# Optimization experiments

Hardware: AMD Instinct MI355X
Metric: run time of the kernel (lower is better)

Reference implementation:

```python
import jax, jax.numpy as jnp
import numpy as np

B, S, D_MODEL = 2, 2048, 2048
H, KVH, HD = 32, 8, 64
N_REP = H // KVH
EPS = 1e-6


def _rope_tables(seq_len, head_dim):
    pos = np.arange(seq_len, dtype=np.float32)
    inv_freq = 1.0 / (10000.0 ** (np.arange(0, head_dim, 2, dtype=np.float32) / head_dim))
    freqs = pos[:, None] * inv_freq[None, :]           # [S, HD/2]
    emb = np.concatenate([freqs, freqs], axis=-1)      # [S, HD]
    return jnp.asarray(np.cos(emb)), jnp.asarray(np.sin(emb))


def setup_inputs() -> dict:
    key = jax.random.key(0)
    ks = jax.random.split(key, 6)
    x = jax.random.normal(ks[0], (B, S, D_MODEL), jnp.float32)
    rope_cos, rope_sin = _rope_tables(S, HD)
    sc_in = 1.0 / np.sqrt(D_MODEL).astype(np.float32)
    sc_o = 1.0 / np.sqrt(H * HD).astype(np.float32)
    Wq = jax.random.normal(ks[1], (H * HD, D_MODEL), jnp.float32) * sc_in
    Wk = jax.random.normal(ks[2], (KVH * HD, D_MODEL), jnp.float32) * sc_in
    Wv = jax.random.normal(ks[3], (KVH * HD, D_MODEL), jnp.float32) * sc_in
    Wo = jax.random.normal(ks[4], (D_MODEL, H * HD), jnp.float32) * sc_o
    q_norm_w = jnp.ones((HD,), jnp.float32)
    k_norm_w = jnp.ones((HD,), jnp.float32)
    return dict(x=x, rope_cos=rope_cos, rope_sin=rope_sin, Wq=Wq, Wk=Wk, Wv=Wv,
                Wo=Wo, q_norm_w=q_norm_w, k_norm_w=k_norm_w)


def _rms_norm(x, w):
    return x * jax.lax.rsqrt(jnp.mean(x * x, axis=-1, keepdims=True) + EPS) * w


def _rotate_half(x):
    x1, x2 = jnp.split(x, 2, axis=-1)
    return jnp.concatenate((-x2, x1), axis=-1)


def reference(x, rope_cos, rope_sin, Wq, Wk, Wv, Wo, q_norm_w, k_norm_w):
    b, s, _ = x.shape
    q = (x @ Wq.T).reshape(b, s, H, HD)
    k = (x @ Wk.T).reshape(b, s, KVH, HD)
    v = (x @ Wv.T).reshape(b, s, KVH, HD)
    # per-head QK RMSNorm
    q = _rms_norm(q, q_norm_w)
    k = _rms_norm(k, k_norm_w)
    # RoPE: cos/sin [S, HD] -> broadcast over heads
    cos = rope_cos[:, None, :]
    sin = rope_sin[:, None, :]
    q = q * cos + _rotate_half(q) * sin
    k = k * cos + _rotate_half(k) * sin
    # GQA: repeat_interleave KV heads
    k = jnp.repeat(k, N_REP, axis=2)
    v = jnp.repeat(v, N_REP, axis=2)
    q = q.transpose(0, 2, 1, 3)  # [B,H,S,HD]
    k = k.transpose(0, 2, 1, 3)
    v = v.transpose(0, 2, 1, 3)
    scale = np.float32(1.0 / np.sqrt(HD))
    scores = jnp.einsum('bhqd,bhkd->bhqk', q, k) * scale
    causal = jnp.tril(jnp.ones((s, s), dtype=bool))
    scores = jnp.where(causal, scores, jnp.finfo(scores.dtype).min)
    attn = jax.nn.softmax(scores, axis=-1)
    out = jnp.einsum('bhqk,bhkd->bhqd', attn, v)
    out = out.transpose(0, 2, 1, 3).reshape(b, s, H * HD)
    return out @ Wo.T
```

## Files before the change

kernel.cpp:

```cpp
#include <hip/hip_runtime.h>
#include <stdint.h>

#define B_ 2
#define S_ 2048
#define DM_ 2048
#define H_ 32
#define KVH_ 8
#define HD_ 64
#define NQK_ 3072

typedef unsigned short u16;
typedef unsigned int u32;
typedef __attribute__((ext_vector_type(8))) short bf16x8;
typedef __attribute__((ext_vector_type(4))) float f32x4;

static __device__ __forceinline__ u16 f2bf(float f) {
  unsigned int u = __float_as_uint(f);
  u = (u + 0x7fffu + ((u >> 16) & 1u)) >> 16;
  return (u16)u;
}
static __device__ __forceinline__ float bf2f(u16 v) {
  unsigned int u = ((unsigned int)v) << 16;
  return __uint_as_float(u);
}

static __device__ __forceinline__ void gload16(const void* g, void* lds_wave_base) {
  __builtin_amdgcn_global_load_lds(
      (__attribute__((address_space(1))) unsigned int*)(uintptr_t)g,
      (__attribute__((address_space(3))) unsigned int*)(uintptr_t)lds_wave_base,
      16, 0, 0);
}

__global__ void cvt_bf16(const float* __restrict__ in, u16* __restrict__ out, int n4) {
  int i = blockIdx.x * blockDim.x + threadIdx.x;
  if (i >= n4) return;
  const float4 v = ((const float4*)in)[i];
  ushort4 o;
  o.x = f2bf(v.x); o.y = f2bf(v.y); o.z = f2bf(v.z); o.w = f2bf(v.w);
  ((ushort4*)out)[i] = o;
}

#define BM 128
#define BN 128
#define BK 32

#define GEMM_BODY(CSTORE)                                                       \
  __shared__ u16 As[2][BM * BK];                                                \
  __shared__ u16 Bs[2][BN * BK];                                                \
  const int t = threadIdx.x;                                                    \
  const int lane = t & 63;                                                      \
  const int w = t >> 6;                                                         \
  const int wr = (w >> 1) * 64, wc = (w & 1) * 64;                              \
  const int m0 = blockIdx.y * BM;                                               \
  const int n0 = blockIdx.x * BN;                                               \
  f32x4 acc[4][4] = {};                                                         \
  const char* Ab = (const char*)A;                                              \
  const char* Bb = (const char*)Bw;                                             \
  const size_t K2 = (size_t)K * 2;                                              \
  const int P0 = t * 16;                                                        \
  const int row0 = P0 >> 6, kb0 = P0 & 63;                                      \
  const int P1 = 4096 + t * 16;                                                 \
  const int row1 = P1 >> 6, kb1 = P1 & 63;                                      \
  const int Pb0 = (w << 10), Pb1 = 4096 + (w << 10);                            \
  auto STAGE = [&](int buf, int k0) {                                           \
    gload16(Ab + (size_t)(m0 + row0) * K2 + (size_t)k0 * 2 + kb0, (char*)As[buf] + Pb0); \
    gload16(Ab + (size_t)(m0 + row1) * K2 + (size_t)k0 * 2 + kb1, (char*)As[buf] + Pb1); \
    gload16(Bb + (size_t)(n0 + row0) * K2 + (size_t)k0 * 2 + kb0, (char*)Bs[buf] + Pb0); \
    gload16(Bb + (size_t)(n0 + row1) * K2 + (size_t)k0 * 2 + kb1, (char*)Bs[buf] + Pb1); \
  };                                                                            \
  STAGE(0, 0);                                                                  \
  __syncthreads();                                                              \
  int cur = 0;                                                                  \
  for (int k0 = 0; k0 < K; k0 += BK) {                                          \
    if (k0 + BK < K) STAGE(cur ^ 1, k0 + BK);                                   \
    bf16x8 af[4], bfr[4];                                                       \
    _Pragma("unroll")                                                           \
    for (int m = 0; m < 4; m++)                                                 \
      af[m] = *(const bf16x8*)((const char*)As[cur] +                           \
               (wr + m * 16 + (lane & 15)) * 64 + ((lane >> 4) << 4));          \
    _Pragma("unroll")                                                           \
    for (int n = 0; n < 4; n++)                                                 \
      bfr[n] = *(const bf16x8*)((const char*)Bs[cur] +                          \
               (wc + n * 16 + (lane & 15)) * 64 + ((lane >> 4) << 4));          \
    _Pragma("unroll")                                                           \
    for (int m = 0; m < 4; m++)                                                 \
      _Pragma("unroll")                                                         \
      for (int n = 0; n < 4; n++)                                               \
        acc[m][n] = __builtin_amdgcn_mfma_f32_16x16x32_bf16(af[m], bfr[n], acc[m][n], 0, 0, 0); \
    __syncthreads();                                                            \
    cur ^= 1;                                                                   \
  }                                                                             \
  _Pragma("unroll")                                                             \
  for (int m = 0; m < 4; m++) {                                                 \
    const int r0 = m0 + wr + m * 16 + ((lane >> 4) << 2);                       \
    _Pragma("unroll")                                                           \
    for (int n = 0; n < 4; n++) {                                               \
      const int c = n0 + wc + n * 16 + (lane & 15);                             \
      _Pragma("unroll")                                                         \
      for (int j = 0; j < 4; j++) CSTORE;                                       \
    }                                                                           \
  }

__global__ __launch_bounds__(256) void gemm_bt(const u16* __restrict__ A,
                                               const u16* __restrict__ Bw,
                                               float* __restrict__ C,
                                               int M, int N, int K) {
  GEMM_BODY(C[(size_t)(r0 + j) * N + c] = acc[m][n][j])
}

__global__ __launch_bounds__(256) void gemm_btb(const u16* __restrict__ A,
                                                const u16* __restrict__ Bw,
                                                u16* __restrict__ C,
                                                int M, int N, int K) {
  GEMM_BODY(C[(size_t)(r0 + j) * N + c] = f2bf(acc[m][n][j]))
}

__global__ void norm_rope_inplace(u16* __restrict__ QKV, const float* __restrict__ cosT,
                                  const float* __restrict__ sinT,
                                  const float* __restrict__ qw,
                                  const float* __restrict__ kw, float qscale) {
  const int r = blockIdx.x * 4 + (threadIdx.x >> 6);
  const int lane = threadIdx.x & 63;
  const int hh2 = r % 40;
  const int bs = r / 40;
  const int s = bs & (S_ - 1);
  const bool isq = hh2 < 32;
  u16* p = QKV + (size_t)bs * NQK_ + hh2 * 64 + lane;
  float x = bf2f(*p);
  float ss = x * x;
#pragma unroll
  for (int m = 1; m < 64; m <<= 1) ss += __shfl_xor(ss, m, 64);
  const float wgt = isq ? qw[lane] : kw[lane];
  float xn = x * rsqrtf(ss * (1.0f / 64.0f) + 1e-6f) * wgt;
  float pr = __shfl_xor(xn, 32, 64);
  float o = xn * cosT[s * 64 + lane] + (lane < 32 ? -pr : pr) * sinT[s * 64 + lane];
  *p = f2bf(o * (isq ? qscale : 1.0f));
}

__global__ void v_transpose(const u16* __restrict__ QKV, u16* __restrict__ Vt) {
  __shared__ u16 tile[64][72];
  const int s0 = blockIdx.x * 64;
  const int bk = blockIdx.y;
  const int b = bk / KVH_, kvh = bk % KVH_;
  const int t = threadIdx.x;
#pragma unroll
  for (int it = 0; it < 16; it++) {
    int idx = it * 256 + t;
    int sl = idx >> 6, d = idx & 63;
    tile[sl][d] = QKV[(size_t)(b * S_ + s0 + sl) * NQK_ + 2560 + kvh * 64 + d];
  }
  __syncthreads();
#pragma unroll
  for (int it = 0; it < 16; it++) {
    int idx = it * 256 + t;
    int d = idx >> 6, sl = idx & 63;
    Vt[(((size_t)(b * KVH_ + kvh)) * HD_ + d) * S_ + s0 + sl] = tile[sl][d];
  }
}

__global__ __launch_bounds__(256, 4) void attn_fwd(const u16* __restrict__ QKV,
                                                   const u16* __restrict__ Vt,
                                                   u16* __restrict__ Out) {
  __shared__ u16 Ksm[2][64 * 64];
  __shared__ u16 Vsm[2][64 * 64];
  __shared__ u16 Psm[4][16 * 64];

  const int t = threadIdx.x, lane = t & 63, w = t >> 6;
  const int q = lane & 15, g = lane >> 4;

  const int fid = blockIdx.y * 16 + blockIdx.x;
  const int xcd = fid & 7, slot = fid >> 3;
  const int kg = xcd * 2 + (slot >> 6);
  const int sub = slot & 63;
  const int ip = sub >> 2;
  const int b = kg >> 3, kvh = kg & 7;
  const int h = kvh * 4 + (sub & 3);

  const char* Kb = (const char*)(QKV + (size_t)b * S_ * NQK_ + 2048 + kvh * 64);
  const char* Vb = (const char*)(Vt + ((size_t)(b * KVH_ + kvh)) * HD_ * S_);

  const int SP0 = t * 16, SP1 = 4096 + t * 16;
  const int srow0 = SP0 >> 7, scb0 = (SP0 ^ ((srow0 & 7) << 4)) & 127;
  const int srow1 = SP1 >> 7, scb1 = (SP1 ^ ((srow1 & 7) << 4)) & 127;
  const int SB0 = (w << 10), SB1 = 4096 + (w << 10);
  const size_t KROW = (size_t)NQK_ * 2;

  auto STAGE = [&](int buf, int kt) {
    gload16(Kb + (size_t)(kt * 64 + srow0) * KROW + scb0, (char*)Ksm[buf] + SB0);
    gload16(Kb + (size_t)(kt * 64 + srow1) * KROW + scb1, (char*)Ksm[buf] + SB1);
    gload16(Vb + (size_t)srow0 * (S_ * 2) + (size_t)kt * 128 + scb0, (char*)Vsm[buf] + SB0);
    gload16(Vb + (size_t)srow1 * (S_ * 2) + (size_t)kt * 128 + scb1, (char*)Vsm[buf] + SB1);
  };

  const int swz = (q & 7) << 4;
  int koff[4][2], voff[4][2], pwoff[4][2], proff[2];
#pragma unroll
  for (int nt = 0; nt < 4; nt++)
#pragma unroll
    for (int hh = 0; hh < 2; hh++) {
      koff[nt][hh] = ((nt * 16 + q) * 128 + hh * 64 + g * 16) ^ swz;
      voff[nt][hh] = ((nt * 16 + q) * 128 + hh * 64 + g * 16) ^ swz;
      pwoff[nt][hh] = (q * 128 + nt * 32 + g * 8 + hh * 4) ^ swz;
    }
#pragma unroll
  for (int c = 0; c < 2; c++) proff[c] = (q * 128 + c * 64 + g * 16) ^ swz;

  bf16x8 ones;
#pragma unroll
  for (int j = 0; j < 8; j++) ones[j] = (short)0x3F80;

  auto process = [&](int qt) {
    const int q0w = qt * 64 + w * 16;
    bf16x8 aq[2];
    {
      const u16* qp = QKV + (size_t)(b * S_ + q0w + q) * NQK_ + h * 64 + g * 8;
      aq[0] = *(const bf16x8*)qp;
      aq[1] = *(const bf16x8*)(qp + 32);
    }
    f32x4 o_acc[4] = {};
    f32x4 l_acc = {};
    float m_i = -1e30f;

    STAGE(0, 0);
    __syncthreads();
    int cur = 0;

    for (int kt = 0; kt <= qt; kt++) {
      if (kt < qt) STAGE(cur ^ 1, kt + 1);

      f32x4 sc[4];
      __builtin_amdgcn_s_setprio(1);
#pragma unroll
      for (int nt = 0; nt < 4; nt++) {
        f32x4 s = {};
#pragma unroll
        for (int hh = 0; hh < 2; hh++) {
          bf16x8 bk = *(const bf16x8*)((const char*)Ksm[cur] + koff[nt][hh]);
          s = __builtin_amdgcn_mfma_f32_16x16x32_bf16(bk, aq[hh], s, 0, 0, 0);
        }
        sc[nt] = s;
      }
      __builtin_amdgcn_s_setprio(0);

      if (kt == qt) {
#pragma unroll
        for (int nt = 0; nt < 4; nt++)
#pragma unroll
          for (int r = 0; r < 4; r++)
            if (nt * 16 + g * 4 + r > w * 16 + q) sc[nt][r] = -1e30f;
      }

      float mx;
      {
        float m0 = fmaxf(fmaxf(sc[0][0], sc[0][1]), fmaxf(sc[0][2], sc[0][3]));
        float m1 = fmaxf(fmaxf(sc[1][0], sc[1][1]), fmaxf(sc[1][2], sc[1][3]));
        float m2 = fmaxf(fmaxf(sc[2][0], sc[2][1]), fmaxf(sc[2][2], sc[2][3]));
        float m3 = fmaxf(fmaxf(sc[3][0], sc[3][1]), fmaxf(sc[3][2], sc[3][3]));
        mx = fmaxf(fmaxf(m0, m1), fmaxf(m2, m3));
      }
      mx = fmaxf(mx, __shfl_xor(mx, 16, 64));
      mx = fmaxf(mx, __shfl_xor(mx, 32, 64));

      if (!__all(mx <= m_i + 8.0f)) {
        const float mn = fmaxf(m_i, mx);
        const float a = exp2f(m_i - mn);
        m_i = mn;
        float aT[4];
#pragma unroll
        for (int r = 0; r < 4; r++)
          aT[r] = __shfl(a, (lane & 48) + ((lane & 48) >> 2) + r, 64);
#pragma unroll
        for (int r = 0; r < 4; r++) {
          l_acc[r] *= aT[r];
#pragma unroll
          for (int dt = 0; dt < 4; dt++) o_acc[dt][r] *= aT[r];
        }
      }

#pragma unroll
      for (int nt = 0; nt < 4; nt++)
#pragma unroll
        for (int r = 0; r < 4; r++) sc[nt][r] = exp2f(sc[nt][r] - m_i);
#pragma unroll
      for (int nt = 0; nt < 4; nt++)
#pragma unroll
        for (int hh = 0; hh < 2; hh++) {
          u32 wv;
          asm("v_cvt_pk_bf16_f32 %0, %1, %2"
              : "=v"(wv) : "v"(sc[nt][2 * hh]), "v"(sc[nt][2 * hh + 1]));
          *(u32*)((char*)Psm[w] + pwoff[nt][hh]) = wv;
        }

      asm volatile("s_waitcnt lgkmcnt(0)" ::: "memory");
      __builtin_amdgcn_sched_barrier(0);

      bf16x8 pa[2];
#pragma unroll
      for (int c = 0; c < 2; c++)
        pa[c] = *(const bf16x8*)((const char*)Psm[w] + proff[c]);

      __builtin_amdgcn_s_setprio(1);
      l_acc = __builtin_amdgcn_mfma_f32_16x16x32_bf16(pa[0], ones, l_acc, 0, 0, 0);
      l_acc = __builtin_amdgcn_mfma_f32_16x16x32_bf16(pa[1], ones, l_acc, 0, 0, 0);
#pragma unroll
      for (int c = 0; c < 2; c++)
#pragma unroll
        for (int dt = 0; dt < 4; dt++) {
          bf16x8 bv = *(const bf16x8*)((const char*)Vsm[cur] + voff[dt][c]);
          o_acc[dt] = __builtin_amdgcn_mfma_f32_16x16x32_bf16(pa[c], bv, o_acc[dt], 0, 0, 0);
        }
      __builtin_amdgcn_s_setprio(0);

      __syncthreads();
      cur ^= 1;
    }

#pragma unroll
    for (int r = 0; r < 4; r++) {
      const int qg = q0w + g * 4 + r;
      const float inv = 1.0f / l_acc[r];
#pragma unroll
      for (int dt = 0; dt < 4; dt++)
        Out[(((size_t)b * S_ + qg) * H_ + h) * HD_ + dt * 16 + q] =
            f2bf(o_acc[dt][r] * inv);
    }
  };

  process(ip);
  process(31 - ip);
}

extern "C" void kernel_launch(void* const* d_in, const int* in_sizes, int n_in,
                              void* d_out, int out_size, void* d_ws, size_t ws_size,
                              hipStream_t stream) {
  const float* x  = (const float*)d_in[0];
  const float* rc = (const float*)d_in[1];
  const float* rs = (const float*)d_in[2];
  const float* Wq = (const float*)d_in[3];
  const float* Wk = (const float*)d_in[4];
  const float* Wv = (const float*)d_in[5];
  const float* Wo = (const float*)d_in[6];
  const float* qw = (const float*)d_in[7];
  const float* kw = (const float*)d_in[8];
  float* out = (float*)d_out;

  char* ws = (char*)d_ws;
  const size_t MB = (size_t)1 << 20;
  u16* xb   = (u16*)(ws + 0 * MB);
  u16* wbq  = (u16*)(ws + 16 * MB);
  u16* QKVb = (u16*)(ws + 28 * MB);
  u16* Vtb  = (u16*)(ws + 52 * MB);
  u16* AO   = xb;

  const int MT = B_ * S_;
  const float QSC = 0.125f * 1.44269504089f;

  cvt_bf16<<<dim3(MT * DM_ / 1024), 256, 0, stream>>>(x, xb, MT * DM_ / 4);
  cvt_bf16<<<dim3(DM_ * DM_ / 1024), 256, 0, stream>>>(Wq, wbq, DM_ * DM_ / 4);
  cvt_bf16<<<dim3(512 * DM_ / 1024), 256, 0, stream>>>(Wk, wbq + (size_t)DM_ * DM_, 512 * DM_ / 4);
  cvt_bf16<<<dim3(512 * DM_ / 1024), 256, 0, stream>>>(Wv, wbq + (size_t)DM_ * DM_ + (size_t)512 * DM_, 512 * DM_ / 4);

  gemm_btb<<<dim3(NQK_ / BN, MT / BM), 256, 0, stream>>>(xb, wbq, QKVb, MT, NQK_, DM_);

  norm_rope_inplace<<<dim3(MT * 40 / 4), 256, 0, stream>>>(QKVb, rc, rs, qw, kw, QSC);

  v_transpose<<<dim3(S_ / 64, B_ * KVH_), 256, 0, stream>>>(QKVb, Vtb);

  attn_fwd<<<dim3(16, 64), 256, 0, stream>>>(QKVb, Vtb, AO);

  cvt_bf16<<<dim3(DM_ * DM_ / 1024), 256, 0, stream>>>(Wo, wbq, DM_ * DM_ / 4);
  gemm_bt<<<dim3(DM_ / BN, MT / BM), 256, 0, stream>>>(AO, wbq, out, MT, DM_, DM_);
}
```

Before: 240.1 us.

## Fuse QK RMSNorm and RoPE into QKV GEMM epilogue; merge conversion kernels

Moves the per-head RMSNorm, RoPE and Q scaling into the epilogue of the QKV projection GEMM. The 16 lanes sharing a row reduce the 64-wide head with shuffles, which removes the separate in-place norm_rope kernel and its extra bf16 read/write of Q and K. The five fp32-to-bf16 conversion launches are merged into one grid-stride kernel, with Wo converted into its own buffer up front instead of reusing the Wq buffer later. This trades fewer launches and less memory traffic for a heavier GEMM epilogue with strided cos/sin loads.

```diff
diff --git a/kernel.cpp b/kernel.cpp
--- a/kernel.cpp
+++ b/kernel.cpp
@@ -19,10 +19,6 @@
   u = (u + 0x7fffu + ((u >> 16) & 1u)) >> 16;
   return (u16)u;
 }
-static __device__ __forceinline__ float bf2f(u16 v) {
-  unsigned int u = ((unsigned int)v) << 16;
-  return __uint_as_float(u);
-}
 
 static __device__ __forceinline__ void gload16(const void* g, void* lds_wave_base) {
   __builtin_amdgcn_global_load_lds(
@@ -31,25 +27,39 @@
       16, 0, 0);
 }
 
-__global__ void cvt_bf16(const float* __restrict__ in, u16* __restrict__ out, int n4) {
-  int i = blockIdx.x * blockDim.x + threadIdx.x;
-  if (i >= n4) return;
-  const float4 v = ((const float4*)in)[i];
-  ushort4 o;
-  o.x = f2bf(v.x); o.y = f2bf(v.y); o.z = f2bf(v.z); o.w = f2bf(v.w);
-  ((ushort4*)out)[i] = o;
+__global__ void cvt_all(const float* __restrict__ x, const float* __restrict__ wq,
+                        const float* __restrict__ wk, const float* __restrict__ wv,
+                        const float* __restrict__ wo,
+                        u16* __restrict__ xb, u16* __restrict__ wbq,
+                        u16* __restrict__ wbo) {
+  const int NX = 2097152, NQ = 1048576, NKV = 262144;
+  const int TOT = NX + NQ + 2 * NKV + NQ;
+  const int stride = gridDim.x * 256;
+  for (int i = blockIdx.x * 256 + threadIdx.x; i < TOT; i += stride) {
+    const float4* s; ushort4* d; int off;
+    if (i < NX)                { s = (const float4*)x;  d = (ushort4*)xb;  off = i; }
+    else if (i < NX + NQ)      { s = (const float4*)wq; d = (ushort4*)wbq; off = i - NX; }
+    else if (i < NX + NQ + NKV){ s = (const float4*)wk; d = (ushort4*)(wbq + (size_t)DM_ * DM_); off = i - NX - NQ; }
+    else if (i < NX + NQ + 2 * NKV) { s = (const float4*)wv; d = (ushort4*)(wbq + (size_t)DM_ * DM_ + (size_t)512 * DM_); off = i - NX - NQ - NKV; }
+    else                       { s = (const float4*)wo; d = (ushort4*)wbo; off = i - NX - NQ - 2 * NKV; }
+    const float4 v = s[off];
+    ushort4 o;
+    o.x = f2bf(v.x); o.y = f2bf(v.y); o.z = f2bf(v.z); o.w = f2bf(v.w);
+    d[off] = o;
+  }
 }
 
 #define BM 128
 #define BN 128
 #define BK 32
 
-#define GEMM_BODY(CSTORE)                                                       \
+#define GEMM_MAIN                                                               \
   __shared__ u16 As[2][BM * BK];                                                \
   __shared__ u16 Bs[2][BN * BK];                                                \
   const int t = threadIdx.x;                                                    \
   const int lane = t & 63;                                                      \
   const int w = t >> 6;                                                         \
+  const int q = lane & 15, g = lane >> 4;                                       \
   const int wr = (w >> 1) * 64, wc = (w & 1) * 64;                              \
   const int m0 = blockIdx.y * BM;                                               \
   const int n0 = blockIdx.x * BN;                                               \
@@ -77,11 +87,11 @@
     _Pragma("unroll")                                                           \
     for (int m = 0; m < 4; m++)                                                 \
       af[m] = *(const bf16x8*)((const char*)As[cur] +                           \
-               (wr + m * 16 + (lane & 15)) * 64 + ((lane >> 4) << 4));          \
+               (wr + m * 16 + q) * 64 + (g << 4));                              \
     _Pragma("unroll")                                                           \
     for (int n = 0; n < 4; n++)                                                 \
       bfr[n] = *(const bf16x8*)((const char*)Bs[cur] +                          \
-               (wc + n * 16 + (lane & 15)) * 64 + ((lane >> 4) << 4));          \
+               (wc + n * 16 + q) * 64 + (g << 4));                              \
     _Pragma("unroll")                                                           \
     for (int m = 0; m < 4; m++)                                                 \
       _Pragma("unroll")                                                         \
@@ -89,52 +99,77 @@
         acc[m][n] = __builtin_amdgcn_mfma_f32_16x16x32_bf16(af[m], bfr[n], acc[m][n], 0, 0, 0); \
     __syncthreads();                                                            \
     cur ^= 1;                                                                   \
-  }                                                                             \
-  _Pragma("unroll")                                                             \
-  for (int m = 0; m < 4; m++) {                                                 \
-    const int r0 = m0 + wr + m * 16 + ((lane >> 4) << 2);                       \
-    _Pragma("unroll")                                                           \
-    for (int n = 0; n < 4; n++) {                                               \
-      const int c = n0 + wc + n * 16 + (lane & 15);                             \
-      _Pragma("unroll")                                                         \
-      for (int j = 0; j < 4; j++) CSTORE;                                       \
-    }                                                                           \
   }
 
 __global__ __launch_bounds__(256) void gemm_bt(const u16* __restrict__ A,
                                                const u16* __restrict__ Bw,
                                                float* __restrict__ C,
                                                int M, int N, int K) {
-  GEMM_BODY(C[(size_t)(r0 + j) * N + c] = acc[m][n][j])
-}
-
-__global__ __launch_bounds__(256) void gemm_btb(const u16* __restrict__ A,
+  GEMM_MAIN
+#pragma unroll
+  for (int m = 0; m < 4; m++) {
+    const int r0 = m0 + wr + m * 16 + g * 4;
+#pragma unroll
+    for (int n = 0; n < 4; n++) {
+      const int c = n0 + wc + n * 16 + q;
+#pragma unroll
+      for (int j = 0; j < 4; j++)
+        C[(size_t)(r0 + j) * N + c] = acc[m][n][j];
+    }
+  }
+}
+
+__global__ __launch_bounds__(256) void gemm_qkv(const u16* __restrict__ A,
                                                 const u16* __restrict__ Bw,
                                                 u16* __restrict__ C,
+                                                const float* __restrict__ cosT,
+                                                const float* __restrict__ sinT,
+                                                const float* __restrict__ qwv,
+                                                const float* __restrict__ kwv,
+                                                float qscale,
                                                 int M, int N, int K) {
-  GEMM_BODY(C[(size_t)(r0 + j) * N + c] = f2bf(acc[m][n][j]))
-}
-
-__global__ void norm_rope_inplace(u16* __restrict__ QKV, const float* __restrict__ cosT,
-                                  const float* __restrict__ sinT,
-                                  const float* __restrict__ qw,
-                                  const float* __restrict__ kw, float qscale) {
-  const int r = blockIdx.x * 4 + (threadIdx.x >> 6);
-  const int lane = threadIdx.x & 63;
-  const int hh2 = r % 40;
-  const int bs = r / 40;
-  const int s = bs & (S_ - 1);
-  const bool isq = hh2 < 32;
-  u16* p = QKV + (size_t)bs * NQK_ + hh2 * 64 + lane;
-  float x = bf2f(*p);
-  float ss = x * x;
-#pragma unroll
-  for (int m = 1; m < 64; m <<= 1) ss += __shfl_xor(ss, m, 64);
-  const float wgt = isq ? qw[lane] : kw[lane];
-  float xn = x * rsqrtf(ss * (1.0f / 64.0f) + 1e-6f) * wgt;
-  float pr = __shfl_xor(xn, 32, 64);
-  float o = xn * cosT[s * 64 + lane] + (lane < 32 ? -pr : pr) * sinT[s * 64 + lane];
-  *p = f2bf(o * (isq ? qscale : 1.0f));
+  GEMM_MAIN
+  const int hcol = (n0 + wc) >> 6;
+  const bool isV = hcol >= 40;
+  const bool isQ = hcol < 32;
+  const float osc = isQ ? qscale : 1.0f;
+  float wgt[4] = {1.f, 1.f, 1.f, 1.f};
+  if (!isV) {
+    const float* wp = isQ ? qwv : kwv;
+#pragma unroll
+    for (int n = 0; n < 4; n++) wgt[n] = wp[n * 16 + q];
+  }
+#pragma unroll
+  for (int m = 0; m < 4; m++) {
+#pragma unroll
+    for (int j = 0; j < 4; j++) {
+      const int row = m0 + wr + m * 16 + g * 4 + j;
+      float v[4];
+#pragma unroll
+      for (int n = 0; n < 4; n++) v[n] = acc[m][n][j];
+      if (!isV) {
+        float ss = v[0] * v[0] + v[1] * v[1] + v[2] * v[2] + v[3] * v[3];
+        ss += __shfl_xor(ss, 1, 64);
+        ss += __shfl_xor(ss, 2, 64);
+        ss += __shfl_xor(ss, 4, 64);
+        ss += __shfl_xor(ss, 8, 64);
+        const float inv = rsqrtf(ss * (1.0f / 64.0f) + 1e-6f);
+        const int s = row & (S_ - 1);
+        float xn[4];
+#pragma unroll
+        for (int n = 0; n < 4; n++) xn[n] = v[n] * inv * wgt[n];
+#pragma unroll
+        for (int n = 0; n < 4; n++) {
+          const float rot = (n < 2) ? -xn[n + 2] : xn[n - 2];
+          const int d = n * 16 + q;
+          v[n] = (xn[n] * cosT[s * 64 + d] + rot * sinT[s * 64 + d]) * osc;
+        }
+      }
+#pragma unroll
+      for (int n = 0; n < 4; n++)
+        C[(size_t)row * N + (n0 + wc + n * 16 + q)] = f2bf(v[n]);
+    }
+  }
 }
 
 __global__ void v_transpose(const u16* __restrict__ QKV, u16* __restrict__ Vt) {
@@ -348,26 +383,22 @@
   const size_t MB = (size_t)1 << 20;
   u16* xb   = (u16*)(ws + 0 * MB);
   u16* wbq  = (u16*)(ws + 16 * MB);
-  u16* QKVb = (u16*)(ws + 28 * MB);
-  u16* Vtb  = (u16*)(ws + 52 * MB);
+  u16* wbo  = (u16*)(ws + 28 * MB);
+  u16* QKVb = (u16*)(ws + 36 * MB);
+  u16* Vtb  = (u16*)(ws + 60 * MB);
   u16* AO   = xb;
 
   const int MT = B_ * S_;
   const float QSC = 0.125f * 1.44269504089f;
 
-  cvt_bf16<<<dim3(MT * DM_ / 1024), 256, 0, stream>>>(x, xb, MT * DM_ / 4);
-  cvt_bf16<<<dim3(DM_ * DM_ / 1024), 256, 0, stream>>>(Wq, wbq, DM_ * DM_ / 4);
-  cvt_bf16<<<dim3(512 * DM_ / 1024), 256, 0, stream>>>(Wk, wbq + (size_t)DM_ * DM_, 512 * DM_ / 4);
-  cvt_bf16<<<dim3(512 * DM_ / 1024), 256, 0, stream>>>(Wv, wbq + (size_t)DM_ * DM_ + (size_t)512 * DM_, 512 * DM_ / 4);
-
-  gemm_btb<<<dim3(NQK_ / BN, MT / BM), 256, 0, stream>>>(xb, wbq, QKVb, MT, NQK_, DM_);
-
-  norm_rope_inplace<<<dim3(MT * 40 / 4), 256, 0, stream>>>(QKVb, rc, rs, qw, kw, QSC);
+  cvt_all<<<dim3(2048), 256, 0, stream>>>(x, Wq, Wk, Wv, Wo, xb, wbq, wbo);
+
+  gemm_qkv<<<dim3(NQK_ / BN, MT / BM), 256, 0, stream>>>(
+      xb, wbq, QKVb, rc, rs, qw, kw, QSC, MT, NQK_, DM_);
 
   v_transpose<<<dim3(S_ / 64, B_ * KVH_), 256, 0, stream>>>(QKVb, Vtb);
 
   attn_fwd<<<dim3(16, 64), 256, 0, stream>>>(QKVb, Vtb, AO);
 
-  cvt_bf16<<<dim3(DM_ * DM_ / 1024), 256, 0, stream>>>(Wo, wbq, DM_ * DM_ / 4);
-  gemm_bt<<<dim3(DM_ / BN, MT / BM), 256, 0, stream>>>(AO, wbq, out, MT, DM_, DM_);
-}
+  gemm_bt<<<dim3(DM_ / BN, MT / BM), 256, 0, stream>>>(AO, wbo, out, MT, DM_, DM_);
+}
```

Measured after the change: 216.4 us. 9.9% less time.
